# Kernel tuning notes

Measured on AMD Instinct MI355X. Metric: run time of the kernel, lower is better.

The kernel has to match this reference:

```python
import jax, jax.numpy as jnp
import numpy as np

B, N, F, H, N_ITERS = 64, 256, 16, 256, 10


def setup_inputs() -> dict:
    key = jax.random.key(0)
    ks = jax.random.split(key, 20)
    s = 0.05
    jets = jax.random.normal(ks[0], (B, N, F), dtype=jnp.float32)
    # row-normalized dense adjacency (D^-1 A style)
    a = jax.random.uniform(ks[1], (B, N, N), dtype=jnp.float32)
    dads = a / jnp.sum(a, axis=-1, keepdims=True)
    p = lambda k, sh: jax.random.normal(k, sh, dtype=jnp.float32) * s
    return {
        'jets': jets, 'dads': dads,
        'W_emb': p(ks[2], (F, H)), 'b_emb': jnp.zeros((H,), jnp.float32),
        'W_msg': p(ks[3], (H, H)), 'b_msg': jnp.zeros((H,), jnp.float32),
        # GRU vertex update: input = concat(message[H], s[F]) -> H
        'Wz': p(ks[4], (H + F, H)), 'Uz': p(ks[5], (H, H)), 'bz': jnp.zeros((H,), jnp.float32),
        'Wr': p(ks[6], (H + F, H)), 'Ur': p(ks[7], (H, H)), 'br': jnp.zeros((H,), jnp.float32),
        'Wh': p(ks[8], (H + F, H)), 'Uh': p(ks[9], (H, H)), 'bh': jnp.zeros((H,), jnp.float32),
        'W_r1': p(ks[10], (H, H)), 'b_r1': jnp.zeros((H,), jnp.float32),
        'W_r2': p(ks[11], (H, H)), 'b_r2': jnp.zeros((H,), jnp.float32),
    }


def reference(jets, dads, W_emb, b_emb, W_msg, b_msg,
              Wz, Uz, bz, Wr, Ur, br, Wh, Uh, bh,
              W_r1, b_r1, W_r2, b_r2):
    # Embedding: [B,N,F] -> [B,N,H]
    h = jnp.tanh(jets @ W_emb + b_emb)
    for _ in range(N_ITERS):
        # Message: linear then adjacency aggregation + tanh
        m = jnp.tanh(jnp.matmul(dads, h @ W_msg + b_msg))  # [B,N,H]
        # GRU-style vertex update; input = concat(message, original features s)
        x = jnp.concatenate([m, jets], axis=-1)            # [B,N,H+F]
        z = jax.nn.sigmoid(x @ Wz + h @ Uz + bz)
        r = jax.nn.sigmoid(x @ Wr + h @ Ur + br)
        h_tilde = jnp.tanh(x @ Wh + (r * h) @ Uh + bh)
        h = (1.0 - z) * h + z * h_tilde
    # Readout: per-node MLP then sum over nodes -> [B,H]
    out = jnp.sum(jnp.tanh(h @ W_r1 + b_r1) @ W_r2 + b_r2, axis=1)
    return out
```

## Files before the change

### kernel.cpp

```cpp
#include <hip/hip_runtime.h>

#define DEVI __device__ __forceinline__

typedef __attribute__((ext_vector_type(4))) float f32x4;
typedef __attribute__((ext_vector_type(8))) short s16x8;
typedef __attribute__((ext_vector_type(4))) short s16x4;
typedef unsigned short u16;
typedef unsigned int u32;

#define WST 288
#define SROW 264
#define AST 260

#define WAITVM(n) __builtin_amdgcn_s_waitcnt(((n)&0xF) | 0x70 | 0xF00 | (((n)>>4)<<14))

DEVI u16 f2bf(float x){
  u32 u = __float_as_uint(x);
  u = (u + 0x7fffu + ((u >> 16) & 1u)) >> 16;
  return (u16)u;
}
DEVI float bf2f(u16 v){ return __uint_as_float(((u32)v) << 16); }

DEVI float fsigm(float x){ return __builtin_amdgcn_rcpf(1.f + __builtin_amdgcn_exp2f(-1.442695041f * x)); }
DEVI float ftanh(float x){ float e = __builtin_amdgcn_exp2f(2.885390082f * x); return 1.f - 2.f * __builtin_amdgcn_rcpf(e + 1.f); }

DEVI s16x8 ld8(const u16* p){ return *(const s16x8*)p; }
DEVI s16x8 ldb64p(const u16* p){
  s16x4 lo = *(const s16x4*)p;
  s16x4 hi = *(const s16x4*)(p + 4);
  s16x8 r;
  r[0]=lo[0]; r[1]=lo[1]; r[2]=lo[2]; r[3]=lo[3];
  r[4]=hi[0]; r[5]=hi[1]; r[6]=hi[2]; r[7]=hi[3];
  return r;
}

DEVI f32x4 ld4bf(const u16* p){
  uint2 v = *(const uint2*)p;
  f32x4 r;
  r[0] = bf2f((u16)(v.x & 0xffff)); r[1] = bf2f((u16)(v.x >> 16));
  r[2] = bf2f((u16)(v.y & 0xffff)); r[3] = bf2f((u16)(v.y >> 16));
  return r;
}

DEVI void st4bf(u16* p, float a, float b, float c, float d){
  uint2 v;
  v.x = (u32)f2bf(a) | ((u32)f2bf(b) << 16);
  v.y = (u32)f2bf(c) | ((u32)f2bf(d) << 16);
  *(uint2*)p = v;
}

#define MFMA(a,b,c) __builtin_amdgcn_mfma_f32_16x16x32_bf16((a),(b),(c),0,0,0)

DEVI void dma4(const u16* lanebase, int rowStrideElems, int c, u16* ldsbase){
#pragma unroll
  for(int q = 0; q < 4; q++){
    const u16* g = lanebase + (size_t)q*16*rowStrideElems + c*32;
    __builtin_amdgcn_global_load_lds((__attribute__((address_space(1))) const void*)g,
                                     (__attribute__((address_space(3))) void*)(ldsbase + q*512),
                                     16, 0, 0);
  }
}
#define AFRAG(buf, t) ld8(&(buf)[(t)*512 + ln*32 + ((qd ^ ((ln>>1)&3))*8)])

__global__ void k_prep(
  const float* __restrict__ jets, const float* __restrict__ dads, const float* __restrict__ W_emb,
  const float* __restrict__ W_msg, const float* __restrict__ Wz, const float* __restrict__ Uz,
  const float* __restrict__ Wr, const float* __restrict__ Ur, const float* __restrict__ Wh,
  const float* __restrict__ Uh, const float* __restrict__ W_r1,
  u16* __restrict__ jp, u16* __restrict__ dadsb, u16* __restrict__ Wet, u16* __restrict__ Wmt,
  u16* __restrict__ Wzt, u16* __restrict__ Uzt, u16* __restrict__ Wrt, u16* __restrict__ Urt,
  u16* __restrict__ Wht, u16* __restrict__ Uht, u16* __restrict__ Wr1t)
{
  int blk = blockIdx.x, tid = threadIdx.x;
  if(blk < 1280){
    int mi = blk >> 8, k = blk & 255, j = tid;
    const float* src; u16* dst;
    switch(mi){
      case 0: src = W_msg; dst = Wmt;  break;
      case 1: src = Uz;    dst = Uzt;  break;
      case 2: src = Ur;    dst = Urt;  break;
      case 3: src = Uh;    dst = Uht;  break;
      default: src = W_r1; dst = Wr1t; break;
    }
    dst[j*256 + k] = f2bf(src[k*256 + j]);
  } else if(blk < 2144){
    int q = blk - 1280; int mi = q / 288; int k = q - mi*288; int j = tid;
    const float* src; u16* dst;
    switch(mi){ case 0: src = Wz; dst = Wzt; break; case 1: src = Wr; dst = Wrt; break; default: src = Wh; dst = Wht; break; }
    dst[j*WST + k] = (k < 272) ? f2bf(src[k*256 + j]) : (u16)0;
  } else if(blk < 2176){
    int idx = (blk - 2144)*256 + tid;
    int j = idx >> 5, k = idx & 31;
    Wet[idx] = (k < 16) ? f2bf(W_emb[k*256 + j]) : (u16)0;
  } else if(blk < 4224){
    int idx = (blk - 2176)*256 + tid;
    int n = idx >> 5, k = idx & 31;
    jp[idx] = (k < 16) ? f2bf(jets[n*16 + k]) : (u16)0;
  } else {
    int idx = (blk - 4224)*256 + tid;
    f32x4 v = *(const f32x4*)(dads + (size_t)idx*4);
    st4bf(dadsb + (size_t)idx*4, v[0], v[1], v[2], v[3]);
  }
}

__global__ __launch_bounds__(256,3) void k_embed(
  u16* __restrict__ h, u16* __restrict__ hmo,
  const u16* __restrict__ jp, const u16* __restrict__ Wet, const float* __restrict__ be,
  const u16* __restrict__ Wmt, const float* __restrict__ bm)
{
  __shared__ u16 hbuf[16*SROW];
  const int tid = threadIdx.x;
  const int wv = tid >> 6, lane = tid & 63, ln = lane & 15, qd = lane >> 4;
  const int n0 = blockIdx.x * 16;
  const int b  = n0 >> 8;
  const int nb = n0 & 255;
  const int nodeA = n0 + ln;

  s16x8 jfr = ld8(jp + (size_t)nodeA*32 + qd*8);
#pragma unroll
  for(int t = 0; t < 4; t++){
    int j0 = (wv*4 + t) * 16;
    f32x4 acc = {0.f,0.f,0.f,0.f};
    s16x8 a = ld8(Wet + (size_t)(j0 + ln)*32 + qd*8);
    acc = MFMA(a, jfr, acc);
    f32x4 bv = *(const f32x4*)(be + j0 + qd*4);
    f32x4 hv;
#pragma unroll
    for(int r = 0; r < 4; r++) hv[r] = ftanh(acc[r] + bv[r]);
    st4bf(h + (size_t)nodeA*256 + j0 + qd*4, hv[0], hv[1], hv[2], hv[3]);
    st4bf(&hbuf[ln*SROW + j0 + qd*4], hv[0], hv[1], hv[2], hv[3]);
  }
  __syncthreads();

  s16x8 af[8];
#pragma unroll
  for(int c = 0; c < 8; c++) af[c] = ld8(&hbuf[ln*SROW + c*32 + qd*8]);
#pragma unroll
  for(int tp = 0; tp < 2; tp++){
    int j0 = (wv*4 + tp*2) * 16, j1 = j0 + 16;
    f32x4 a0 = {0.f,0.f,0.f,0.f}, a1 = {0.f,0.f,0.f,0.f};
#pragma unroll
    for(int c = 0; c < 8; c++){
      a0 = MFMA(af[c], ld8(Wmt + (size_t)(j0 + ln)*256 + c*32 + qd*8), a0);
      a1 = MFMA(af[c], ld8(Wmt + (size_t)(j1 + ln)*256 + c*32 + qd*8), a1);
    }
    float b0 = bm[j0 + ln], b1 = bm[j1 + ln];
    st4bf(hmo + (size_t)(b*256 + j0 + ln)*256 + nb + qd*4, a0[0]+b0, a0[1]+b0, a0[2]+b0, a0[3]+b0);
    st4bf(hmo + (size_t)(b*256 + j1 + ln)*256 + nb + qd*4, a1[0]+b1, a1[1]+b1, a1[2]+b1, a1[3]+b1);
  }
}

__global__ __launch_bounds__(256,1) void k_gru(
  u16* __restrict__ h,
  const u16* __restrict__ hmi, u16* __restrict__ hmo,
  const u16* __restrict__ dadsb, const u16* __restrict__ jp,
  const u16* __restrict__ Wzt, const u16* __restrict__ Wrt, const u16* __restrict__ Wht,
  const u16* __restrict__ Uzt, const u16* __restrict__ Urt, const u16* __restrict__ Uht,
  const u16* __restrict__ Wmt,
  const float* __restrict__ bz, const float* __restrict__ br, const float* __restrict__ bhb,
  const float* __restrict__ bm)
{
  __shared__ u16 smM[64*AST];
  __shared__ u16 smB[64*AST];
  __shared__ __align__(16) u16 stg[4][2][2][2048];
  const int tid = threadIdx.x;
  const int wv = tid >> 6, lane = tid & 63, ln = lane & 15, qd = lane >> 4;
  const int blk   = blockIdx.x;
  const int batch = (blk & 7) * 8 + (blk >> 5);
  const int group = (blk >> 3) & 3;
  const int n0 = batch * 256 + group * 64;
  const int b  = batch;
  const int nb = group * 64;
  const int j0w = wv * 64;

  u16* s0 = &stg[wv][0][0][0];
  u16* s1 = &stg[wv][1][0][0];
  u16* u0 = &stg[wv][0][1][0];
  u16* u1 = &stg[wv][1][1][0];

  const int rw = lane >> 2;
  const int cs = ((lane & 3) ^ ((lane >> 3) & 3)) * 8;

  const u16* laneA = hmi + (size_t)(b*256 + j0w + rw)*256 + cs;
  dma4(laneA, 256, 0, s0);

  s16x8 jB[4];
#pragma unroll
  for(int i = 0; i < 4; i++) jB[i] = ld8(jp + (size_t)(n0 + i*16 + ln)*32 + qd*8);

  {
    f32x4 acc[4][4];
#pragma unroll
    for(int t = 0; t < 4; t++)
#pragma unroll
      for(int i = 0; i < 4; i++) acc[t][i] = (f32x4){0.f,0.f,0.f,0.f};
    s16x8 Bf[4], Bn[4];
#pragma unroll
    for(int i = 0; i < 4; i++) Bf[i] = ld8(dadsb + (size_t)(n0 + i*16 + ln)*256 + qd*8);
#pragma unroll
    for(int c = 0; c < 8; c++){
      u16* cur = (c & 1) ? s1 : s0;
      if(c < 7){
        dma4(laneA, 256, c+1, (c & 1) ? s0 : s1);
#pragma unroll
        for(int i = 0; i < 4; i++) Bn[i] = ld8(dadsb + (size_t)(n0 + i*16 + ln)*256 + (c+1)*32 + qd*8);
        WAITVM(8);
      } else {
        WAITVM(0);
      }
#pragma unroll
      for(int t = 0; t < 4; t++){
        s16x8 A = AFRAG(cur, t);
#pragma unroll
        for(int i = 0; i < 4; i++) acc[t][i] = MFMA(A, Bf[i], acc[t][i]);
      }
      if(c < 7){
#pragma unroll
        for(int i = 0; i < 4; i++) Bf[i] = Bn[i];
      }
    }
#pragma unroll
    for(int t = 0; t < 4; t++)
#pragma unroll
      for(int i = 0; i < 4; i++)
        st4bf(&smM[(i*16 + ln)*AST + j0w + t*16 + qd*4],
              ftanh(acc[t][i][0]), ftanh(acc[t][i][1]), ftanh(acc[t][i][2]), ftanh(acc[t][i][3]));
  }
  const u16* laneWr = Wrt + (size_t)(j0w + rw)*WST + cs;
  const u16* laneUr = Urt + (size_t)(j0w + rw)*256 + cs;
  dma4(laneWr, WST, 0, s0);
  dma4(laneUr, 256, 0, u0);
  __syncthreads();

  {
    f32x4 acc[4][4];
#pragma unroll
    for(int t = 0; t < 4; t++)
#pragma unroll
      for(int i = 0; i < 4; i++) acc[t][i] = (f32x4){0.f,0.f,0.f,0.f};
    s16x8 Aj[4];
#pragma unroll
    for(int t = 0; t < 4; t++) Aj[t] = ld8(Wrt + (size_t)(j0w + t*16 + ln)*WST + 256 + qd*8);
    s16x8 Bh[4], Bn[4];
#pragma unroll
    for(int i = 0; i < 4; i++) Bh[i] = ld8(h + (size_t)(n0 + i*16 + ln)*256 + qd*8);
#pragma unroll
    for(int c = 0; c < 8; c++){
      u16* cw = (c & 1) ? s1 : s0;
      u16* cu = (c & 1) ? u1 : u0;
      if(c < 7){
        dma4(laneWr, WST, c+1, (c & 1) ? s0 : s1);
        dma4(laneUr, 256, c+1, (c & 1) ? u0 : u1);
#pragma unroll
        for(int i = 0; i < 4; i++) Bn[i] = ld8(h + (size_t)(n0 + i*16 + ln)*256 + (c+1)*32 + qd*8);
        WAITVM(12);
      } else {
        WAITVM(0);
      }
      s16x8 Bm[4];
#pragma unroll
      for(int i = 0; i < 4; i++) Bm[i] = ldb64p(&smM[(i*16 + ln)*AST + c*32 + qd*8]);
#pragma unroll
      for(int t = 0; t < 4; t++){
        s16x8 Aw = AFRAG(cw, t);
#pragma unroll
        for(int i = 0; i < 4; i++) acc[t][i] = MFMA(Aw, Bm[i], acc[t][i]);
      }
#pragma unroll
      for(int t = 0; t < 4; t++){
        s16x8 Au = AFRAG(cu, t);
#pragma unroll
        for(int i = 0; i < 4; i++) acc[t][i] = MFMA(Au, Bh[i], acc[t][i]);
      }
      if(c < 7){
#pragma unroll
        for(int i = 0; i < 4; i++) Bh[i] = Bn[i];
      }
    }
#pragma unroll
    for(int t = 0; t < 4; t++)
#pragma unroll
      for(int i = 0; i < 4; i++) acc[t][i] = MFMA(Aj[t], jB[i], acc[t][i]);
#pragma unroll
    for(int t = 0; t < 4; t++){
      f32x4 bv = *(const f32x4*)(br + j0w + t*16 + qd*4);
#pragma unroll
      for(int i = 0; i < 4; i++){
        f32x4 hv = ld4bf(h + (size_t)(n0 + i*16 + ln)*256 + j0w + t*16 + qd*4);
        st4bf(&smB[(i*16 + ln)*AST + j0w + t*16 + qd*4],
              fsigm(acc[t][i][0]+bv[0])*hv[0], fsigm(acc[t][i][1]+bv[1])*hv[1],
              fsigm(acc[t][i][2]+bv[2])*hv[2], fsigm(acc[t][i][3]+bv[3])*hv[3]);
      }
    }
  }
  const u16* laneWz = Wzt + (size_t)(j0w + rw)*WST + cs;
  const u16* laneUz = Uzt + (size_t)(j0w + rw)*256 + cs;
  dma4(laneWz, WST, 0, s0);
  dma4(laneUz, 256, 0, u0);
  __syncthreads();

  f32x4 zacc[4][4], gacc[4][4];
#pragma unroll
  for(int t = 0; t < 4; t++)
#pragma unroll
    for(int i = 0; i < 4; i++) zacc[t][i] = (f32x4){0.f,0.f,0.f,0.f};
  {
    s16x8 Aj[4];
#pragma unroll
    for(int t = 0; t < 4; t++) Aj[t] = ld8(Wzt + (size_t)(j0w + t*16 + ln)*WST + 256 + qd*8);
    s16x8 Bh[4], Bn[4];
#pragma unroll
    for(int i = 0; i < 4; i++) Bh[i] = ld8(h + (size_t)(n0 + i*16 + ln)*256 + qd*8);
#pragma unroll
    for(int c = 0; c < 8; c++){
      u16* cw = (c & 1) ? s1 : s0;
      u16* cu = (c & 1) ? u1 : u0;
      if(c < 7){
        dma4(laneWz, WST, c+1, (c & 1) ? s0 : s1);
        dma4(laneUz, 256, c+1, (c & 1) ? u0 : u1);
#pragma unroll
        for(int i = 0; i < 4; i++) Bn[i] = ld8(h + (size_t)(n0 + i*16 + ln)*256 + (c+1)*32 + qd*8);
        WAITVM(12);
      } else {
        WAITVM(0);
      }
      s16x8 Bm[4];
#pragma unroll
      for(int i = 0; i < 4; i++) Bm[i] = ldb64p(&smM[(i*16 + ln)*AST + c*32 + qd*8]);
#pragma unroll
      for(int t = 0; t < 4; t++){
        s16x8 Aw = AFRAG(cw, t);
#pragma unroll
        for(int i = 0; i < 4; i++) zacc[t][i] = MFMA(Aw, Bm[i], zacc[t][i]);
      }
#pragma unroll
      for(int t = 0; t < 4; t++){
        s16x8 Au = AFRAG(cu, t);
#pragma unroll
        for(int i = 0; i < 4; i++) zacc[t][i] = MFMA(Au, Bh[i], zacc[t][i]);
      }
      if(c < 7){
#pragma unroll
        for(int i = 0; i < 4; i++) Bh[i] = Bn[i];
      }
    }
#pragma unroll
    for(int t = 0; t < 4; t++)
#pragma unroll
      for(int i = 0; i < 4; i++) zacc[t][i] = MFMA(Aj[t], jB[i], zacc[t][i]);
  }

  const u16* laneWh = Wht + (size_t)(j0w + rw)*WST + cs;
  const u16* laneUh = Uht + (size_t)(j0w + rw)*256 + cs;
  dma4(laneWh, WST, 0, s0);
  dma4(laneUh, 256, 0, u0);

#pragma unroll
  for(int t = 0; t < 4; t++)
#pragma unroll
    for(int i = 0; i < 4; i++) gacc[t][i] = (f32x4){0.f,0.f,0.f,0.f};
  {
    s16x8 Aj[4];
#pragma unroll
    for(int t = 0; t < 4; t++) Aj[t] = ld8(Wht + (size_t)(j0w + t*16 + ln)*WST + 256 + qd*8);
#pragma unroll
    for(int c = 0; c < 8; c++){
      u16* cw = (c & 1) ? s1 : s0;
      u16* cu = (c & 1) ? u1 : u0;
      if(c < 7){
        dma4(laneWh, WST, c+1, (c & 1) ? s0 : s1);
        dma4(laneUh, 256, c+1, (c & 1) ? u0 : u1);
        WAITVM(8);
      } else {
        WAITVM(0);
      }
      s16x8 Bm[4], Brh[4];
#pragma unroll
      for(int i = 0; i < 4; i++){
        Bm[i]  = ldb64p(&smM[(i*16 + ln)*AST + c*32 + qd*8]);
        Brh[i] = ldb64p(&smB[(i*16 + ln)*AST + c*32 + qd*8]);
      }
#pragma unroll
      for(int t = 0; t < 4; t++){
        s16x8 Aw = AFRAG(cw, t);
#pragma unroll
        for(int i = 0; i < 4; i++) gacc[t][i] = MFMA(Aw, Bm[i], gacc[t][i]);
      }
#pragma unroll
      for(int t = 0; t < 4; t++){
        s16x8 Au = AFRAG(cu, t);
#pragma unroll
        for(int i = 0; i < 4; i++) gacc[t][i] = MFMA(Au, Brh[i], gacc[t][i]);
      }
    }
#pragma unroll
    for(int t = 0; t < 4; t++)
#pragma unroll
      for(int i = 0; i < 4; i++) gacc[t][i] = MFMA(Aj[t], jB[i], gacc[t][i]);
  }
  __syncthreads();

#pragma unroll
  for(int t = 0; t < 4; t++){
    f32x4 bzv = *(const f32x4*)(bz + j0w + t*16 + qd*4);
    f32x4 bhv = *(const f32x4*)(bhb + j0w + t*16 + qd*4);
#pragma unroll
    for(int i = 0; i < 4; i++){
      f32x4 hv = ld4bf(h + (size_t)(n0 + i*16 + ln)*256 + j0w + t*16 + qd*4);
      f32x4 hn;
#pragma unroll
      for(int r = 0; r < 4; r++){
        float z  = fsigm(zacc[t][i][r] + bzv[r]);
        float th = ftanh(gacc[t][i][r] + bhv[r]);
        hn[r] = hv[r] + z * (th - hv[r]);
      }
      st4bf(h + (size_t)(n0 + i*16 + ln)*256 + j0w + t*16 + qd*4, hn[0], hn[1], hn[2], hn[3]);
      st4bf(&smM[(i*16 + ln)*AST + j0w + t*16 + qd*4], hn[0], hn[1], hn[2], hn[3]);
    }
  }
  const u16* laneWm = Wmt + (size_t)(j0w + rw)*256 + cs;
  dma4(laneWm, 256, 0, s0);
  __syncthreads();

  {
    f32x4 acc[4][4];
#pragma unroll
    for(int t = 0; t < 4; t++)
#pragma unroll
      for(int i = 0; i < 4; i++) acc[t][i] = (f32x4){0.f,0.f,0.f,0.f};
#pragma unroll
    for(int c = 0; c < 8; c++){
      u16* cur = (c & 1) ? s1 : s0;
      if(c < 7){
        dma4(laneWm, 256, c+1, (c & 1) ? s0 : s1);
        WAITVM(4);
      } else {
        WAITVM(0);
      }
      s16x8 Bf[4];
#pragma unroll
      for(int i = 0; i < 4; i++) Bf[i] = ldb64p(&smM[(i*16 + ln)*AST + c*32 + qd*8]);
#pragma unroll
      for(int t = 0; t < 4; t++){
        s16x8 A = AFRAG(cur, t);
#pragma unroll
        for(int i = 0; i < 4; i++) acc[t][i] = MFMA(A, Bf[i], acc[t][i]);
      }
    }
#pragma unroll
    for(int t = 0; t < 4; t++){
      f32x4 bmv = *(const f32x4*)(bm + j0w + t*16 + qd*4);
#pragma unroll
      for(int i = 0; i < 4; i++){
#pragma unroll
        for(int r = 0; r < 4; r++){
          hmo[(size_t)(b*256 + j0w + t*16 + qd*4 + r)*256 + nb + i*16 + ln] =
            f2bf(acc[t][i][r] + bmv[r]);
        }
      }
    }
  }
}

__global__ __launch_bounds__(256,3) void k_t(
  const u16* __restrict__ h, u16* __restrict__ t_out,
  const u16* __restrict__ Wr1t, const float* __restrict__ br1)
{
  const int tid = threadIdx.x;
  const int wv = tid >> 6, lane = tid & 63, ln = lane & 15, qd = lane >> 4;
  const int n0 = blockIdx.x * 16;
  const int nodeA = n0 + ln;

  s16x8 hfr[8];
#pragma unroll
  for(int c = 0; c < 8; c++) hfr[c] = ld8(h + (size_t)nodeA*256 + c*32 + qd*8);
#pragma unroll
  for(int tp = 0; tp < 2; tp++){
    int j0 = (wv*4 + tp*2) * 16, j1 = j0 + 16;
    f32x4 a0 = {0.f,0.f,0.f,0.f}, a1 = {0.f,0.f,0.f,0.f};
#pragma unroll
    for(int c = 0; c < 8; c++){
      a0 = MFMA(ld8(Wr1t + (size_t)(j0 + ln)*256 + c*32 + qd*8), hfr[c], a0);
      a1 = MFMA(ld8(Wr1t + (size_t)(j1 + ln)*256 + c*32 + qd*8), hfr[c], a1);
    }
    f32x4 b0 = *(const f32x4*)(br1 + j0 + qd*4);
    f32x4 b1 = *(const f32x4*)(br1 + j1 + qd*4);
    st4bf(t_out + (size_t)nodeA*256 + j0 + qd*4,
          ftanh(a0[0]+b0[0]), ftanh(a0[1]+b0[1]), ftanh(a0[2]+b0[2]), ftanh(a0[3]+b0[3]));
    st4bf(t_out + (size_t)nodeA*256 + j1 + qd*4,
          ftanh(a1[0]+b1[0]), ftanh(a1[1]+b1[1]), ftanh(a1[2]+b1[2]), ftanh(a1[3]+b1[3]));
  }
}

__global__ void k_red(const u16* __restrict__ t, const float* __restrict__ W_r2,
                      const float* __restrict__ b_r2, float* __restrict__ out){
  __shared__ float s[256];
  int b = blockIdx.x, k = threadIdx.x;
  float acc = 0.f;
  for(int n = 0; n < 256; n++) acc += bf2f(t[(size_t)(b*256 + n)*256 + k]);
  s[k] = acc;
  __syncthreads();
  int j = threadIdx.x;
  float o = 256.f * b_r2[j];
  for(int k2 = 0; k2 < 256; k2++) o += s[k2] * W_r2[k2*256 + j];
  out[b*256 + j] = o;
}

extern "C" void kernel_launch(void* const* d_in, const int* in_sizes, int n_in,
                              void* d_out, int out_size, void* d_ws, size_t ws_size,
                              hipStream_t stream)
{
  const float* jets  = (const float*)d_in[0];
  const float* dads  = (const float*)d_in[1];
  const float* W_emb = (const float*)d_in[2];
  const float* b_emb = (const float*)d_in[3];
  const float* W_msg = (const float*)d_in[4];
  const float* b_msg = (const float*)d_in[5];
  const float* Wz    = (const float*)d_in[6];
  const float* Uz    = (const float*)d_in[7];
  const float* bz    = (const float*)d_in[8];
  const float* Wr    = (const float*)d_in[9];
  const float* Ur    = (const float*)d_in[10];
  const float* br    = (const float*)d_in[11];
  const float* Wh    = (const float*)d_in[12];
  const float* Uh    = (const float*)d_in[13];
  const float* bh    = (const float*)d_in[14];
  const float* W_r1  = (const float*)d_in[15];
  const float* b_r1  = (const float*)d_in[16];
  const float* W_r2  = (const float*)d_in[17];
  const float* b_r2  = (const float*)d_in[18];

  char* ws = (char*)d_ws;
  u16* h      = (u16*)(ws);
  u16* hmA    = (u16*)(ws + 8388608);
  u16* hmB    = (u16*)(ws + 16777216);
  u16* dadsb  = (u16*)(ws + 25165824);
  u16* jp     = (u16*)(ws + 33554432);
  u16* Wmt    = (u16*)(ws + 34603008);
  u16* Uzt    = (u16*)(ws + 34734080);
  u16* Urt    = (u16*)(ws + 34865152);
  u16* Uht    = (u16*)(ws + 34996224);
  u16* Wr1t   = (u16*)(ws + 35127296);
  u16* Wzt    = (u16*)(ws + 35258368);
  u16* Wrt    = (u16*)(ws + 35405824);
  u16* Wht    = (u16*)(ws + 35553280);
  u16* Wet    = (u16*)(ws + 35700736);
  float* outp = (float*)d_out;

  k_prep<<<8320, 256, 0, stream>>>(jets, dads, W_emb, W_msg, Wz, Uz, Wr, Ur, Wh, Uh, W_r1,
                                   jp, dadsb, Wet, Wmt, Wzt, Uzt, Wrt, Urt, Wht, Uht, Wr1t);
  k_embed<<<1024, 256, 0, stream>>>(h, hmA, jp, Wet, b_emb, Wmt, b_msg);
  for(int it = 0; it < 10; ++it){
    const u16* hin = (it & 1) ? hmB : hmA;
    u16* hout      = (it & 1) ? hmA : hmB;
    k_gru<<<256, 256, 0, stream>>>(h, hin, hout, dadsb, jp,
                                   Wzt, Wrt, Wht, Uzt, Urt, Uht, Wmt,
                                   bz, br, bh, b_msg);
  }
  k_t<<<1024, 256, 0, stream>>>(h, hmB, Wr1t, b_r1);
  k_red<<<64, 256, 0, stream>>>(hmB, W_r2, b_r2, outp);
}
```

Baseline: 561.2 us.

## Triple-buffer DMA weight staging and XOR-swizzle shared activation tiles

Every GEMM stage in the fused GRU kernel moves from double to triple buffering, so the per-wave LDS staging and the register prefetch of dads and h run two chunks ahead, with wait counts adjusted to match. The padded smM/smB arrays (row stride 260) are replaced by unpadded 256-wide rows with an XOR swizzle on the column offset, which saves LDS and is meant to avoid bank conflicts. The aim is to hide more global-load latency behind the MFMA work. In exchange it uses more LDS staging space and more registers, and it carries some risk in the hand-tuned waitcnt values.

```diff
diff --git a/kernel.cpp b/kernel.cpp
--- a/kernel.cpp
+++ b/kernel.cpp
@@ -10,7 +10,6 @@
 
 #define WST 288
 #define SROW 264
-#define AST 260
 
 #define WAITVM(n) __builtin_amdgcn_s_waitcnt(((n)&0xF) | 0x70 | 0xF00 | (((n)>>4)<<14))
 
@@ -25,14 +24,6 @@
 DEVI float ftanh(float x){ float e = __builtin_amdgcn_exp2f(2.885390082f * x); return 1.f - 2.f * __builtin_amdgcn_rcpf(e + 1.f); }
 
 DEVI s16x8 ld8(const u16* p){ return *(const s16x8*)p; }
-DEVI s16x8 ldb64p(const u16* p){
-  s16x4 lo = *(const s16x4*)p;
-  s16x4 hi = *(const s16x4*)(p + 4);
-  s16x8 r;
-  r[0]=lo[0]; r[1]=lo[1]; r[2]=lo[2]; r[3]=lo[3];
-  r[4]=hi[0]; r[5]=hi[1]; r[6]=hi[2]; r[7]=hi[3];
-  return r;
-}
 
 DEVI f32x4 ld4bf(const u16* p){
   uint2 v = *(const uint2*)p;
@@ -47,6 +38,19 @@
   v.x = (u32)f2bf(a) | ((u32)f2bf(b) << 16);
   v.y = (u32)f2bf(c) | ((u32)f2bf(d) << 16);
   *(uint2*)p = v;
+}
+
+DEVI int soff(int row, int off){ return off ^ ((row & 15) << 2); }
+DEVI s16x8 ldsw(const u16* sm, int row, int off){
+  s16x4 lo = *(const s16x4*)&sm[row*256 + soff(row, off)];
+  s16x4 hi = *(const s16x4*)&sm[row*256 + soff(row, off + 4)];
+  s16x8 r;
+  r[0]=lo[0]; r[1]=lo[1]; r[2]=lo[2]; r[3]=lo[3];
+  r[4]=hi[0]; r[5]=hi[1]; r[6]=hi[2]; r[7]=hi[3];
+  return r;
+}
+DEVI void stsw(u16* sm, int row, int off, float a, float b, float c, float d){
+  st4bf(&sm[row*256 + soff(row, off)], a, b, c, d);
 }
 
 #define MFMA(a,b,c) __builtin_amdgcn_mfma_f32_16x16x32_bf16((a),(b),(c),0,0,0)
@@ -160,9 +164,9 @@
   const float* __restrict__ bz, const float* __restrict__ br, const float* __restrict__ bhb,
   const float* __restrict__ bm)
 {
-  __shared__ u16 smM[64*AST];
-  __shared__ u16 smB[64*AST];
-  __shared__ __align__(16) u16 stg[4][2][2][2048];
+  __shared__ u16 smM[64*256];
+  __shared__ u16 smB[64*256];
+  __shared__ __align__(16) u16 stg[4][3][2][2048];
   const int tid = threadIdx.x;
   const int wv = tid >> 6, lane = tid & 63, ln = lane & 15, qd = lane >> 4;
   const int blk   = blockIdx.x;
@@ -173,20 +177,24 @@
   const int nb = group * 64;
   const int j0w = wv * 64;
 
-  u16* s0 = &stg[wv][0][0][0];
-  u16* s1 = &stg[wv][1][0][0];
-  u16* u0 = &stg[wv][0][1][0];
-  u16* u1 = &stg[wv][1][1][0];
+  u16* sb[3] = { &stg[wv][0][0][0], &stg[wv][1][0][0], &stg[wv][2][0][0] };
+  u16* ub[3] = { &stg[wv][0][1][0], &stg[wv][1][1][0], &stg[wv][2][1][0] };
 
   const int rw = lane >> 2;
   const int cs = ((lane & 3) ^ ((lane >> 3) & 3)) * 8;
 
+  s16x8 jB[4];
+#pragma unroll
+  for(int i = 0; i < 4; i++) jB[i] = ld8(jp + (size_t)(n0 + i*16 + ln)*32 + qd*8);
+
   const u16* laneA = hmi + (size_t)(b*256 + j0w + rw)*256 + cs;
-  dma4(laneA, 256, 0, s0);
-
-  s16x8 jB[4];
-#pragma unroll
-  for(int i = 0; i < 4; i++) jB[i] = ld8(jp + (size_t)(n0 + i*16 + ln)*32 + qd*8);
+  s16x8 BD[3][4];
+#pragma unroll
+  for(int i = 0; i < 4; i++) BD[0][i] = ld8(dadsb + (size_t)(n0 + i*16 + ln)*256 + qd*8);
+  dma4(laneA, 256, 0, sb[0]);
+#pragma unroll
+  for(int i = 0; i < 4; i++) BD[1][i] = ld8(dadsb + (size_t)(n0 + i*16 + ln)*256 + 32 + qd*8);
+  dma4(laneA, 256, 1, sb[1]);
 
   {
     f32x4 acc[4][4];
@@ -194,42 +202,44 @@
     for(int t = 0; t < 4; t++)
 #pragma unroll
       for(int i = 0; i < 4; i++) acc[t][i] = (f32x4){0.f,0.f,0.f,0.f};
-    s16x8 Bf[4], Bn[4];
-#pragma unroll
-    for(int i = 0; i < 4; i++) Bf[i] = ld8(dadsb + (size_t)(n0 + i*16 + ln)*256 + qd*8);
-#pragma unroll
-    for(int c = 0; c < 8; c++){
-      u16* cur = (c & 1) ? s1 : s0;
-      if(c < 7){
-        dma4(laneA, 256, c+1, (c & 1) ? s0 : s1);
-#pragma unroll
-        for(int i = 0; i < 4; i++) Bn[i] = ld8(dadsb + (size_t)(n0 + i*16 + ln)*256 + (c+1)*32 + qd*8);
+#pragma unroll
+    for(int c = 0; c < 8; c++){
+      if(c < 6){
+#pragma unroll
+        for(int i = 0; i < 4; i++) BD[(c+2)%3][i] = ld8(dadsb + (size_t)(n0 + i*16 + ln)*256 + (c+2)*32 + qd*8);
+        dma4(laneA, 256, c+2, sb[(c+2)%3]);
+        WAITVM(16);
+      } else if(c == 6){
         WAITVM(8);
       } else {
         WAITVM(0);
       }
 #pragma unroll
       for(int t = 0; t < 4; t++){
-        s16x8 A = AFRAG(cur, t);
-#pragma unroll
-        for(int i = 0; i < 4; i++) acc[t][i] = MFMA(A, Bf[i], acc[t][i]);
-      }
-      if(c < 7){
-#pragma unroll
-        for(int i = 0; i < 4; i++) Bf[i] = Bn[i];
+        s16x8 A = AFRAG(sb[c%3], t);
+#pragma unroll
+        for(int i = 0; i < 4; i++) acc[t][i] = MFMA(A, BD[c%3][i], acc[t][i]);
       }
     }
 #pragma unroll
     for(int t = 0; t < 4; t++)
 #pragma unroll
       for(int i = 0; i < 4; i++)
-        st4bf(&smM[(i*16 + ln)*AST + j0w + t*16 + qd*4],
-              ftanh(acc[t][i][0]), ftanh(acc[t][i][1]), ftanh(acc[t][i][2]), ftanh(acc[t][i][3]));
-  }
+        stsw(smM, i*16 + ln, j0w + t*16 + qd*4,
+             ftanh(acc[t][i][0]), ftanh(acc[t][i][1]), ftanh(acc[t][i][2]), ftanh(acc[t][i][3]));
+  }
+
   const u16* laneWr = Wrt + (size_t)(j0w + rw)*WST + cs;
   const u16* laneUr = Urt + (size_t)(j0w + rw)*256 + cs;
-  dma4(laneWr, WST, 0, s0);
-  dma4(laneUr, 256, 0, u0);
+  s16x8 BH[3][4];
+#pragma unroll
+  for(int i = 0; i < 4; i++) BH[0][i] = ld8(h + (size_t)(n0 + i*16 + ln)*256 + qd*8);
+  dma4(laneWr, WST, 0, sb[0]);
+  dma4(laneUr, 256, 0, ub[0]);
+#pragma unroll
+  for(int i = 0; i < 4; i++) BH[1][i] = ld8(h + (size_t)(n0 + i*16 + ln)*256 + 32 + qd*8);
+  dma4(laneWr, WST, 1, sb[1]);
+  dma4(laneUr, 256, 1, ub[1]);
   __syncthreads();
 
   {
@@ -241,40 +251,33 @@
     s16x8 Aj[4];
 #pragma unroll
     for(int t = 0; t < 4; t++) Aj[t] = ld8(Wrt + (size_t)(j0w + t*16 + ln)*WST + 256 + qd*8);
-    s16x8 Bh[4], Bn[4];
-#pragma unroll
-    for(int i = 0; i < 4; i++) Bh[i] = ld8(h + (size_t)(n0 + i*16 + ln)*256 + qd*8);
-#pragma unroll
-    for(int c = 0; c < 8; c++){
-      u16* cw = (c & 1) ? s1 : s0;
-      u16* cu = (c & 1) ? u1 : u0;
-      if(c < 7){
-        dma4(laneWr, WST, c+1, (c & 1) ? s0 : s1);
-        dma4(laneUr, 256, c+1, (c & 1) ? u0 : u1);
-#pragma unroll
-        for(int i = 0; i < 4; i++) Bn[i] = ld8(h + (size_t)(n0 + i*16 + ln)*256 + (c+1)*32 + qd*8);
+#pragma unroll
+    for(int c = 0; c < 8; c++){
+      if(c < 6){
+#pragma unroll
+        for(int i = 0; i < 4; i++) BH[(c+2)%3][i] = ld8(h + (size_t)(n0 + i*16 + ln)*256 + (c+2)*32 + qd*8);
+        dma4(laneWr, WST, c+2, sb[(c+2)%3]);
+        dma4(laneUr, 256, c+2, ub[(c+2)%3]);
+        WAITVM(24);
+      } else if(c == 6){
         WAITVM(12);
       } else {
         WAITVM(0);
       }
       s16x8 Bm[4];
 #pragma unroll
-      for(int i = 0; i < 4; i++) Bm[i] = ldb64p(&smM[(i*16 + ln)*AST + c*32 + qd*8]);
-#pragma unroll
-      for(int t = 0; t < 4; t++){
-        s16x8 Aw = AFRAG(cw, t);
+      for(int i = 0; i < 4; i++) Bm[i] = ldsw(smM, i*16 + ln, c*32 + qd*8);
+#pragma unroll
+      for(int t = 0; t < 4; t++){
+        s16x8 Aw = AFRAG(sb[c%3], t);
 #pragma unroll
         for(int i = 0; i < 4; i++) acc[t][i] = MFMA(Aw, Bm[i], acc[t][i]);
       }
 #pragma unroll
       for(int t = 0; t < 4; t++){
-        s16x8 Au = AFRAG(cu, t);
-#pragma unroll
-        for(int i = 0; i < 4; i++) acc[t][i] = MFMA(Au, Bh[i], acc[t][i]);
-      }
-      if(c < 7){
-#pragma unroll
-        for(int i = 0; i < 4; i++) Bh[i] = Bn[i];
+        s16x8 Au = AFRAG(ub[c%3], t);
+#pragma unroll
+        for(int i = 0; i < 4; i++) acc[t][i] = MFMA(Au, BH[c%3][i], acc[t][i]);
       }
     }
 #pragma unroll
@@ -287,16 +290,23 @@
 #pragma unroll
       for(int i = 0; i < 4; i++){
         f32x4 hv = ld4bf(h + (size_t)(n0 + i*16 + ln)*256 + j0w + t*16 + qd*4);
-        st4bf(&smB[(i*16 + ln)*AST + j0w + t*16 + qd*4],
-              fsigm(acc[t][i][0]+bv[0])*hv[0], fsigm(acc[t][i][1]+bv[1])*hv[1],
-              fsigm(acc[t][i][2]+bv[2])*hv[2], fsigm(acc[t][i][3]+bv[3])*hv[3]);
-      }
-    }
-  }
+        stsw(smB, i*16 + ln, j0w + t*16 + qd*4,
+             fsigm(acc[t][i][0]+bv[0])*hv[0], fsigm(acc[t][i][1]+bv[1])*hv[1],
+             fsigm(acc[t][i][2]+bv[2])*hv[2], fsigm(acc[t][i][3]+bv[3])*hv[3]);
+      }
+    }
+  }
+
   const u16* laneWz = Wzt + (size_t)(j0w + rw)*WST + cs;
   const u16* laneUz = Uzt + (size_t)(j0w + rw)*256 + cs;
-  dma4(laneWz, WST, 0, s0);
-  dma4(laneUz, 256, 0, u0);
+#pragma unroll
+  for(int i = 0; i < 4; i++) BH[0][i] = ld8(h + (size_t)(n0 + i*16 + ln)*256 + qd*8);
+  dma4(laneWz, WST, 0, sb[0]);
+  dma4(laneUz, 256, 0, ub[0]);
+#pragma unroll
+  for(int i = 0; i < 4; i++) BH[1][i] = ld8(h + (size_t)(n0 + i*16 + ln)*256 + 32 + qd*8);
+  dma4(laneWz, WST, 1, sb[1]);
+  dma4(laneUz, 256, 1, ub[1]);
   __syncthreads();
 
   f32x4 zacc[4][4], gacc[4][4];
@@ -308,40 +318,33 @@
     s16x8 Aj[4];
 #pragma unroll
     for(int t = 0; t < 4; t++) Aj[t] = ld8(Wzt + (size_t)(j0w + t*16 + ln)*WST + 256 + qd*8);
-    s16x8 Bh[4], Bn[4];
-#pragma unroll
-    for(int i = 0; i < 4; i++) Bh[i] = ld8(h + (size_t)(n0 + i*16 + ln)*256 + qd*8);
-#pragma unroll
-    for(int c = 0; c < 8; c++){
-      u16* cw = (c & 1) ? s1 : s0;
-      u16* cu = (c & 1) ? u1 : u0;
-      if(c < 7){
-        dma4(laneWz, WST, c+1, (c & 1) ? s0 : s1);
-        dma4(laneUz, 256, c+1, (c & 1) ? u0 : u1);
-#pragma unroll
-        for(int i = 0; i < 4; i++) Bn[i] = ld8(h + (size_t)(n0 + i*16 + ln)*256 + (c+1)*32 + qd*8);
+#pragma unroll
+    for(int c = 0; c < 8; c++){
+      if(c < 6){
+#pragma unroll
+        for(int i = 0; i < 4; i++) BH[(c+2)%3][i] = ld8(h + (size_t)(n0 + i*16 + ln)*256 + (c+2)*32 + qd*8);
+        dma4(laneWz, WST, c+2, sb[(c+2)%3]);
+        dma4(laneUz, 256, c+2, ub[(c+2)%3]);
+        WAITVM(24);
+      } else if(c == 6){
         WAITVM(12);
       } else {
         WAITVM(0);
       }
       s16x8 Bm[4];
 #pragma unroll
-      for(int i = 0; i < 4; i++) Bm[i] = ldb64p(&smM[(i*16 + ln)*AST + c*32 + qd*8]);
-#pragma unroll
-      for(int t = 0; t < 4; t++){
-        s16x8 Aw = AFRAG(cw, t);
+      for(int i = 0; i < 4; i++) Bm[i] = ldsw(smM, i*16 + ln, c*32 + qd*8);
+#pragma unroll
+      for(int t = 0; t < 4; t++){
+        s16x8 Aw = AFRAG(sb[c%3], t);
 #pragma unroll
         for(int i = 0; i < 4; i++) zacc[t][i] = MFMA(Aw, Bm[i], zacc[t][i]);
       }
 #pragma unroll
       for(int t = 0; t < 4; t++){
-        s16x8 Au = AFRAG(cu, t);
-#pragma unroll
-        for(int i = 0; i < 4; i++) zacc[t][i] = MFMA(Au, Bh[i], zacc[t][i]);
-      }
-      if(c < 7){
-#pragma unroll
-        for(int i = 0; i < 4; i++) Bh[i] = Bn[i];
+        s16x8 Au = AFRAG(ub[c%3], t);
+#pragma unroll
+        for(int i = 0; i < 4; i++) zacc[t][i] = MFMA(Au, BH[c%3][i], zacc[t][i]);
       }
     }
 #pragma unroll
@@ -352,8 +355,10 @@
 
   const u16* laneWh = Wht + (size_t)(j0w + rw)*WST + cs;
   const u16* laneUh = Uht + (size_t)(j0w + rw)*256 + cs;
-  dma4(laneWh, WST, 0, s0);
-  dma4(laneUh, 256, 0, u0);
+  dma4(laneWh, WST, 0, sb[0]);
+  dma4(laneUh, 256, 0, ub[0]);
+  dma4(laneWh, WST, 1, sb[1]);
+  dma4(laneUh, 256, 1, ub[1]);
 
 #pragma unroll
   for(int t = 0; t < 4; t++)
@@ -365,11 +370,11 @@
     for(int t = 0; t < 4; t++) Aj[t] = ld8(Wht + (size_t)(j0w + t*16 + ln)*WST + 256 + qd*8);
 #pragma unroll
     for(int c = 0; c < 8; c++){
-      u16* cw = (c & 1) ? s1 : s0;
-      u16* cu = (c & 1) ? u1 : u0;
-      if(c < 7){
-        dma4(laneWh, WST, c+1, (c & 1) ? s0 : s1);
-        dma4(laneUh, 256, c+1, (c & 1) ? u0 : u1);
+      if(c < 6){
+        dma4(laneWh, WST, c+2, sb[(c+2)%3]);
+        dma4(laneUh, 256, c+2, ub[(c+2)%3]);
+        WAITVM(16);
+      } else if(c == 6){
         WAITVM(8);
       } else {
         WAITVM(0);
@@ -377,18 +382,18 @@
       s16x8 Bm[4], Brh[4];
 #pragma unroll
       for(int i = 0; i < 4; i++){
-        Bm[i]  = ldb64p(&smM[(i*16 + ln)*AST + c*32 + qd*8]);
-        Brh[i] = ldb64p(&smB[(i*16 + ln)*AST + c*32 + qd*8]);
-      }
-#pragma unroll
-      for(int t = 0; t < 4; t++){
-        s16x8 Aw = AFRAG(cw, t);
+        Bm[i]  = ldsw(smM, i*16 + ln, c*32 + qd*8);
+        Brh[i] = ldsw(smB, i*16 + ln, c*32 + qd*8);
+      }
+#pragma unroll
+      for(int t = 0; t < 4; t++){
+        s16x8 Aw = AFRAG(sb[c%3], t);
 #pragma unroll
         for(int i = 0; i < 4; i++) gacc[t][i] = MFMA(Aw, Bm[i], gacc[t][i]);
       }
 #pragma unroll
       for(int t = 0; t < 4; t++){
-        s16x8 Au = AFRAG(cu, t);
+        s16x8 Au = AFRAG(ub[c%3], t);
 #pragma unroll
         for(int i = 0; i < 4; i++) gacc[t][i] = MFMA(Au, Brh[i], gacc[t][i]);
       }
@@ -415,11 +420,12 @@
         hn[r] = hv[r] + z * (th - hv[r]);
       }
       st4bf(h + (size_t)(n0 + i*16 + ln)*256 + j0w + t*16 + qd*4, hn[0], hn[1], hn[2], hn[3]);
-      st4bf(&smM[(i*16 + ln)*AST + j0w + t*16 + qd*4], hn[0], hn[1], hn[2], hn[3]);
+      stsw(smM, i*16 + ln, j0w + t*16 + qd*4, hn[0], hn[1], hn[2], hn[3]);
     }
   }
   const u16* laneWm = Wmt + (size_t)(j0w + rw)*256 + cs;
-  dma4(laneWm, 256, 0, s0);
+  dma4(laneWm, 256, 0, sb[0]);
+  dma4(laneWm, 256, 1, sb[1]);
   __syncthreads();
 
   {
@@ -430,19 +436,20 @@
       for(int i = 0; i < 4; i++) acc[t][i] = (f32x4){0.f,0.f,0.f,0.f};
 #pragma unroll
     for(int c = 0; c < 8; c++){
-      u16* cur = (c & 1) ? s1 : s0;
-      if(c < 7){
-        dma4(laneWm, 256, c+1, (c & 1) ? s0 : s1);
+      if(c < 6){
+        dma4(laneWm, 256, c+2, sb[(c+2)%3]);
+        WAITVM(8);
+      } else if(c == 6){
         WAITVM(4);
       } else {
         WAITVM(0);
       }
       s16x8 Bf[4];
 #pragma unroll
-      for(int i = 0; i < 4; i++) Bf[i] = ldb64p(&smM[(i*16 + ln)*AST + c*32 + qd*8]);
-#pragma unroll
-      for(int t = 0; t < 4; t++){
-        s16x8 A = AFRAG(cur, t);
+      for(int i = 0; i < 4; i++) Bf[i] = ldsw(smM, i*16 + ln, c*32 + qd*8);
+#pragma unroll
+      for(int t = 0; t < 4; t++){
+        s16x8 A = AFRAG(sb[c%3], t);
 #pragma unroll
         for(int i = 0; i < 4; i++) acc[t][i] = MFMA(A, Bf[i], acc[t][i]);
       }
```

Measured after the change: 572.8 us. 1.02x slower.

## Retile embed kernel and fuse readout tanh with node-sum reduction

Applied to the files above, without the earlier changes.

The embedding kernel now processes 64 nodes per block with a 4x4 MFMA register tile, matching the GRU kernel's tiling, so weight fragments are reused across more nodes. The readout fuses the W_r1 matmul, tanh and per-node summation into one kernel that writes partial sums per 64-node group, so the full bf16 intermediate is no longer written and re-read. A wider final kernel then spreads the W_r2 projection over 256 blocks instead of 64. The cost is fewer blocks in the embed and readout kernels and larger register use per thread.

```diff
diff --git a/kernel.cpp b/kernel.cpp
--- a/kernel.cpp
+++ b/kernel.cpp
@@ -9,7 +9,6 @@
 typedef unsigned int u32;
 
 #define WST 288
-#define SROW 264
 #define AST 260
 
 #define WAITVM(n) __builtin_amdgcn_s_waitcnt(((n)&0xF) | 0x70 | 0xF00 | (((n)>>4)<<14))
@@ -103,50 +102,74 @@
   }
 }
 
-__global__ __launch_bounds__(256,3) void k_embed(
+__global__ void k_embed2(
   u16* __restrict__ h, u16* __restrict__ hmo,
   const u16* __restrict__ jp, const u16* __restrict__ Wet, const float* __restrict__ be,
   const u16* __restrict__ Wmt, const float* __restrict__ bm)
 {
-  __shared__ u16 hbuf[16*SROW];
+  __shared__ u16 smM[64*AST];
   const int tid = threadIdx.x;
   const int wv = tid >> 6, lane = tid & 63, ln = lane & 15, qd = lane >> 4;
-  const int n0 = blockIdx.x * 16;
-  const int b  = n0 >> 8;
-  const int nb = n0 & 255;
-  const int nodeA = n0 + ln;
-
-  s16x8 jfr = ld8(jp + (size_t)nodeA*32 + qd*8);
+  const int blk   = blockIdx.x;
+  const int batch = (blk & 7) * 8 + (blk >> 5);
+  const int group = (blk >> 3) & 3;
+  const int n0 = batch * 256 + group * 64;
+  const int b  = batch;
+  const int nb = group * 64;
+  const int j0w = wv * 64;
+
+  s16x8 jB[4];
+#pragma unroll
+  for(int i = 0; i < 4; i++) jB[i] = ld8(jp + (size_t)(n0 + i*16 + ln)*32 + qd*8);
+
 #pragma unroll
   for(int t = 0; t < 4; t++){
-    int j0 = (wv*4 + t) * 16;
-    f32x4 acc = {0.f,0.f,0.f,0.f};
-    s16x8 a = ld8(Wet + (size_t)(j0 + ln)*32 + qd*8);
-    acc = MFMA(a, jfr, acc);
-    f32x4 bv = *(const f32x4*)(be + j0 + qd*4);
-    f32x4 hv;
-#pragma unroll
-    for(int r = 0; r < 4; r++) hv[r] = ftanh(acc[r] + bv[r]);
-    st4bf(h + (size_t)nodeA*256 + j0 + qd*4, hv[0], hv[1], hv[2], hv[3]);
-    st4bf(&hbuf[ln*SROW + j0 + qd*4], hv[0], hv[1], hv[2], hv[3]);
+    s16x8 a = ld8(Wet + (size_t)(j0w + t*16 + ln)*32 + qd*8);
+    f32x4 bv = *(const f32x4*)(be + j0w + t*16 + qd*4);
+#pragma unroll
+    for(int i = 0; i < 4; i++){
+      f32x4 acc = {0.f,0.f,0.f,0.f};
+      acc = MFMA(a, jB[i], acc);
+      f32x4 hv;
+#pragma unroll
+      for(int r = 0; r < 4; r++) hv[r] = ftanh(acc[r] + bv[r]);
+      st4bf(h + (size_t)(n0 + i*16 + ln)*256 + j0w + t*16 + qd*4, hv[0], hv[1], hv[2], hv[3]);
+      st4bf(&smM[(i*16 + ln)*AST + j0w + t*16 + qd*4], hv[0], hv[1], hv[2], hv[3]);
+    }
   }
   __syncthreads();
 
-  s16x8 af[8];
-#pragma unroll
-  for(int c = 0; c < 8; c++) af[c] = ld8(&hbuf[ln*SROW + c*32 + qd*8]);
-#pragma unroll
-  for(int tp = 0; tp < 2; tp++){
-    int j0 = (wv*4 + tp*2) * 16, j1 = j0 + 16;
-    f32x4 a0 = {0.f,0.f,0.f,0.f}, a1 = {0.f,0.f,0.f,0.f};
+  {
+    f32x4 acc[4][4];
+#pragma unroll
+    for(int t = 0; t < 4; t++)
+#pragma unroll
+      for(int i = 0; i < 4; i++) acc[t][i] = (f32x4){0.f,0.f,0.f,0.f};
 #pragma unroll
     for(int c = 0; c < 8; c++){
-      a0 = MFMA(af[c], ld8(Wmt + (size_t)(j0 + ln)*256 + c*32 + qd*8), a0);
-      a1 = MFMA(af[c], ld8(Wmt + (size_t)(j1 + ln)*256 + c*32 + qd*8), a1);
-    }
-    float b0 = bm[j0 + ln], b1 = bm[j1 + ln];
-    st4bf(hmo + (size_t)(b*256 + j0 + ln)*256 + nb + qd*4, a0[0]+b0, a0[1]+b0, a0[2]+b0, a0[3]+b0);
-    st4bf(hmo + (size_t)(b*256 + j1 + ln)*256 + nb + qd*4, a1[0]+b1, a1[1]+b1, a1[2]+b1, a1[3]+b1);
+      s16x8 A[4];
+#pragma unroll
+      for(int t = 0; t < 4; t++) A[t] = ld8(Wmt + (size_t)(j0w + t*16 + ln)*256 + c*32 + qd*8);
+      s16x8 Bf[4];
+#pragma unroll
+      for(int i = 0; i < 4; i++) Bf[i] = ldb64p(&smM[(i*16 + ln)*AST + c*32 + qd*8]);
+#pragma unroll
+      for(int t = 0; t < 4; t++)
+#pragma unroll
+        for(int i = 0; i < 4; i++) acc[t][i] = MFMA(A[t], Bf[i], acc[t][i]);
+    }
+#pragma unroll
+    for(int t = 0; t < 4; t++){
+      f32x4 bmv = *(const f32x4*)(bm + j0w + t*16 + qd*4);
+#pragma unroll
+      for(int i = 0; i < 4; i++){
+#pragma unroll
+        for(int r = 0; r < 4; r++){
+          hmo[(size_t)(b*256 + j0w + t*16 + qd*4 + r)*256 + nb + i*16 + ln] =
+            f2bf(acc[t][i][r] + bmv[r]);
+        }
+      }
+    }
   }
 }
 
@@ -462,48 +485,78 @@
   }
 }
 
-__global__ __launch_bounds__(256,3) void k_t(
-  const u16* __restrict__ h, u16* __restrict__ t_out,
+__global__ void k_tred(
+  const u16* __restrict__ h, float* __restrict__ sred,
   const u16* __restrict__ Wr1t, const float* __restrict__ br1)
 {
   const int tid = threadIdx.x;
   const int wv = tid >> 6, lane = tid & 63, ln = lane & 15, qd = lane >> 4;
-  const int n0 = blockIdx.x * 16;
-  const int nodeA = n0 + ln;
-
-  s16x8 hfr[8];
-#pragma unroll
-  for(int c = 0; c < 8; c++) hfr[c] = ld8(h + (size_t)nodeA*256 + c*32 + qd*8);
-#pragma unroll
-  for(int tp = 0; tp < 2; tp++){
-    int j0 = (wv*4 + tp*2) * 16, j1 = j0 + 16;
-    f32x4 a0 = {0.f,0.f,0.f,0.f}, a1 = {0.f,0.f,0.f,0.f};
-#pragma unroll
-    for(int c = 0; c < 8; c++){
-      a0 = MFMA(ld8(Wr1t + (size_t)(j0 + ln)*256 + c*32 + qd*8), hfr[c], a0);
-      a1 = MFMA(ld8(Wr1t + (size_t)(j1 + ln)*256 + c*32 + qd*8), hfr[c], a1);
-    }
-    f32x4 b0 = *(const f32x4*)(br1 + j0 + qd*4);
-    f32x4 b1 = *(const f32x4*)(br1 + j1 + qd*4);
-    st4bf(t_out + (size_t)nodeA*256 + j0 + qd*4,
-          ftanh(a0[0]+b0[0]), ftanh(a0[1]+b0[1]), ftanh(a0[2]+b0[2]), ftanh(a0[3]+b0[3]));
-    st4bf(t_out + (size_t)nodeA*256 + j1 + qd*4,
-          ftanh(a1[0]+b1[0]), ftanh(a1[1]+b1[1]), ftanh(a1[2]+b1[2]), ftanh(a1[3]+b1[3]));
-  }
-}
-
-__global__ void k_red(const u16* __restrict__ t, const float* __restrict__ W_r2,
-                      const float* __restrict__ b_r2, float* __restrict__ out){
-  __shared__ float s[256];
-  int b = blockIdx.x, k = threadIdx.x;
+  const int blk   = blockIdx.x;
+  const int batch = (blk & 7) * 8 + (blk >> 5);
+  const int group = (blk >> 3) & 3;
+  const int n0 = batch * 256 + group * 64;
+  const int j0w = wv * 64;
+
+  f32x4 acc[4][4];
+#pragma unroll
+  for(int t = 0; t < 4; t++)
+#pragma unroll
+    for(int i = 0; i < 4; i++) acc[t][i] = (f32x4){0.f,0.f,0.f,0.f};
+#pragma unroll
+  for(int c = 0; c < 8; c++){
+    s16x8 A[4];
+#pragma unroll
+    for(int t = 0; t < 4; t++) A[t] = ld8(Wr1t + (size_t)(j0w + t*16 + ln)*256 + c*32 + qd*8);
+    s16x8 Bf[4];
+#pragma unroll
+    for(int i = 0; i < 4; i++) Bf[i] = ld8(h + (size_t)(n0 + i*16 + ln)*256 + c*32 + qd*8);
+#pragma unroll
+    for(int t = 0; t < 4; t++)
+#pragma unroll
+      for(int i = 0; i < 4; i++) acc[t][i] = MFMA(A[t], Bf[i], acc[t][i]);
+  }
+#pragma unroll
+  for(int t = 0; t < 4; t++){
+    f32x4 bv = *(const f32x4*)(br1 + j0w + t*16 + qd*4);
+    f32x4 s = {0.f,0.f,0.f,0.f};
+#pragma unroll
+    for(int i = 0; i < 4; i++)
+#pragma unroll
+      for(int r = 0; r < 4; r++) s[r] += ftanh(acc[t][i][r] + bv[r]);
+#pragma unroll
+    for(int r = 0; r < 4; r++){
+      float v = s[r];
+      v += __shfl_xor(v, 1);
+      v += __shfl_xor(v, 2);
+      v += __shfl_xor(v, 4);
+      v += __shfl_xor(v, 8);
+      s[r] = v;
+    }
+    if(ln == 0){
+      *(f32x4*)&sred[(size_t)(batch*4 + group)*256 + j0w + t*16 + qd*4] = s;
+    }
+  }
+}
+
+__global__ void k_red2(const float* __restrict__ sred, const float* __restrict__ W_r2,
+                       const float* __restrict__ b_r2, float* __restrict__ out){
+  __shared__ float red[4][64];
+  const int blk = blockIdx.x;
+  const int b = blk >> 2, jq = blk & 3;
+  const int jl = threadIdx.x & 63, kq = threadIdx.x >> 6;
+  const int j = jq*64 + jl;
+  const float* s0 = sred + (size_t)b*4*256;
   float acc = 0.f;
-  for(int n = 0; n < 256; n++) acc += bf2f(t[(size_t)(b*256 + n)*256 + k]);
-  s[k] = acc;
+  for(int kk = 0; kk < 64; kk++){
+    int k = kq*64 + kk;
+    float s = s0[k] + s0[256 + k] + s0[512 + k] + s0[768 + k];
+    acc += s * W_r2[(size_t)k*256 + j];
+  }
+  red[kq][jl] = acc;
   __syncthreads();
-  int j = threadIdx.x;
-  float o = 256.f * b_r2[j];
-  for(int k2 = 0; k2 < 256; k2++) o += s[k2] * W_r2[k2*256 + j];
-  out[b*256 + j] = o;
+  if(kq == 0){
+    out[(size_t)b*256 + j] = 256.f * b_r2[j] + red[0][jl] + red[1][jl] + red[2][jl] + red[3][jl];
+  }
 }
 
 extern "C" void kernel_launch(void* const* d_in, const int* in_sizes, int n_in,
@@ -545,11 +598,12 @@
   u16* Wrt    = (u16*)(ws + 35405824);
   u16* Wht    = (u16*)(ws + 35553280);
   u16* Wet    = (u16*)(ws + 35700736);
+  float* sred = (float*)(ws + 16777216);
   float* outp = (float*)d_out;
 
   k_prep<<<8320, 256, 0, stream>>>(jets, dads, W_emb, W_msg, Wz, Uz, Wr, Ur, Wh, Uh, W_r1,
                                    jp, dadsb, Wet, Wmt, Wzt, Uzt, Wrt, Urt, Wht, Uht, Wr1t);
-  k_embed<<<1024, 256, 0, stream>>>(h, hmA, jp, Wet, b_emb, Wmt, b_msg);
+  k_embed2<<<256, 256, 0, stream>>>(h, hmA, jp, Wet, b_emb, Wmt, b_msg);
   for(int it = 0; it < 10; ++it){
     const u16* hin = (it & 1) ? hmB : hmA;
     u16* hout      = (it & 1) ? hmA : hmB;
@@ -557,6 +611,6 @@
                                    Wzt, Wrt, Wht, Uzt, Urt, Uht, Wmt,
                                    bz, br, bh, b_msg);
   }
-  k_t<<<1024, 256, 0, stream>>>(h, hmB, Wr1t, b_r1);
-  k_red<<<64, 256, 0, stream>>>(hmB, W_r2, b_r2, outp);
-}
+  k_tred<<<256, 256, 0, stream>>>(h, sred, Wr1t, b_r1);
+  k_red2<<<256, 256, 0, stream>>>(sred, W_r2, b_r2, outp);
+}
```

After: 535.2 us. 4.6% less time.
